# Performance work log

Hardware: AMD Instinct MI355X
Metric: run time of the kernel (lower is better)

## Reference

```python
import jax, jax.numpy as jnp
import numpy as np

D = 12       # series_dim
L = 1024     # series_length
N = 16       # batch
ADM = 64     # adm_dim
HID = 16     # hidden_size (d_model for gru)
E = 8        # datum_emb_size
OUT = 1      # output_dim
H = HID * D  # GRU hidden per direction = 192
FFH = 512    # PositionWiseFFN hidden


def setup_inputs() -> dict:
    key = jax.random.key(0)
    ks = jax.random.split(key, 20)
    def g(i, shape, s):
        return jax.random.normal(ks[i], shape, jnp.float32) * s
    sh = float(1.0 / np.sqrt(H))
    z = lambda *shape: jnp.zeros(shape, jnp.float32)
    inp = {
        'series': jax.random.normal(ks[0], (N, L, D), jnp.float32),
        'adm': jax.random.normal(ks[1], (N, ADM), jnp.float32),
        'mask': jax.random.randint(ks[2], (N, L, D), 0, 2, jnp.int32),
        'series_W': g(3, (D, E), 1.0),                       # per-channel Linear(1->8), no bias
        'mask_emb': g(4, (D + 1, E), 1.0).at[0].set(0.0),    # padding_idx=0
        'adm_W1': g(5, (HID, ADM), float(1.0 / np.sqrt(ADM))), 'adm_b1': z(HID),
        'adm_W2': g(6, (HID, HID), float(1.0 / np.sqrt(HID))), 'adm_b2': z(HID),
        'Wih0f': g(7, (3 * H, E * D), sh), 'Whh0f': g(8, (3 * H, H), sh), 'bih0f': z(3 * H), 'bhh0f': z(3 * H),
        'Wih0b': g(9, (3 * H, E * D), sh), 'Whh0b': g(10, (3 * H, H), sh), 'bih0b': z(3 * H), 'bhh0b': z(3 * H),
        'Wih1f': g(11, (3 * H, 2 * H), sh), 'Whh1f': g(12, (3 * H, H), sh), 'bih1f': z(3 * H), 'bhh1f': z(3 * H),
        'Wih1b': g(13, (3 * H, 2 * H), sh), 'Whh1b': g(14, (3 * H, H), sh), 'bih1b': z(3 * H), 'bhh1b': z(3 * H),
        'ffn_W1': g(15, (D, FFH, 3 * HID), float(1.0 / np.sqrt(3 * HID))), 'ffn_b1': z(D, FFH),
        'ln_g': jnp.ones((D, FFH), jnp.float32), 'ln_b': z(D, FFH),
        'ffn_W2': g(16, (D, OUT, FFH), float(1.0 / np.sqrt(FFH))), 'ffn_b2': z(D, OUT),
    }
    return inp


def _gru_dir(xp, Whh, bhh, reverse):
    # xp: [N, L, 3H] = x @ W_ih^T + b_ih precomputed for all timesteps
    Hs = Whh.shape[1]
    def step(h, x):
        gh = h @ Whh.T + bhh
        xr, xz, xn = jnp.split(x, 3, axis=-1)
        hr, hz, hn = jnp.split(gh, 3, axis=-1)
        r = jax.nn.sigmoid(xr + hr)
        zg = jax.nn.sigmoid(xz + hz)
        n = jnp.tanh(xn + r * hn)
        hnew = (1.0 - zg) * n + zg * h
        return hnew, hnew
    h0 = jnp.zeros((xp.shape[0], Hs), xp.dtype)
    _, hs = jax.lax.scan(step, h0, jnp.swapaxes(xp, 0, 1), reverse=reverse)
    return jnp.swapaxes(hs, 0, 1)


def reference(series, adm, mask, series_W, mask_emb, adm_W1, adm_b1, adm_W2, adm_b2,
              Wih0f, Whh0f, bih0f, bhh0f, Wih0b, Whh0b, bih0b, bhh0b,
              Wih1f, Whh1f, bih1f, bhh1f, Wih1b, Whh1b, bih1b, bhh1b,
              ffn_W1, ffn_b1, ln_g, ln_b, ffn_W2, ffn_b2):
    n, l, d = series.shape
    # adm MLP (dropouts are identity in eval)
    adm_out = jnp.maximum(adm @ adm_W1.T + adm_b1, 0.0) @ adm_W2.T + adm_b2  # [N, HID]
    # fused per-channel mask-embedding lookup + Linear(1->8) + add
    idx = mask * jnp.arange(1, d + 1, dtype=mask.dtype)          # [N,L,D]
    memb = mask_emb[idx]                                          # [N,L,D,E]
    semb = jnp.einsum('nld,de->nlde', series, series_W)           # [N,L,D,E]
    h = (memb + semb).reshape(n, l, d * E)                        # GRU input [N,L,96]
    # 2-layer bidirectional GRU
    layers = ((Wih0f, Whh0f, bih0f, bhh0f, Wih0b, Whh0b, bih0b, bhh0b),
              (Wih1f, Whh1f, bih1f, bhh1f, Wih1b, Whh1b, bih1b, bhh1b))
    for (Wf, Uf, bif, bhf, Wb, Ub, bib, bhb) in layers:
        fwd = _gru_dir(h @ Wf.T + bif, Uf, bhf, False)
        bwd = _gru_dir(h @ Wb.T + bib, Ub, bhb, True)
        h = jnp.concatenate([fwd, bwd], axis=-1)                  # [N,L,2H]
    # chunk rnn output into D slices of width 2H/D = 32
    r = h.reshape(n, l, d, (2 * H) // d)
    a = jnp.broadcast_to(adm_out[:, None, None, :], (n, l, d, adm_out.shape[-1]))
    feat = jnp.concatenate([r, a], axis=-1)                       # [N,L,D,3*HID]
    # per-channel PositionWiseFFN: Linear -> (Dropout) -> LayerNorm -> ReLU -> Linear
    hh = jnp.einsum('nldk,dhk->nldh', feat, ffn_W1) + ffn_b1      # [N,L,D,FFH]
    mu = hh.mean(axis=-1, keepdims=True)
    var = ((hh - mu) ** 2).mean(axis=-1, keepdims=True)
    hh = (hh - mu) / jnp.sqrt(var + 1e-5) * ln_g + ln_b
    hh = jnp.maximum(hh, 0.0)
    o = jnp.einsum('nldh,doh->nldo', hh, ffn_W2) + ffn_b2         # [N,L,D,OUT]
    return o.reshape(n, l, d * OUT)
```

## Files before the change

### kernel.cpp

```cpp
#include <hip/hip_runtime.h>
#include <math.h>


constexpr int N_   = 16;
constexpr int L_   = 1024;
constexpr int D_   = 12;
constexpr int E_   = 8;
constexpr int HID_ = 16;
constexpr int ADM_ = 64;
constexpr int H_   = 192;
constexpr int H3_  = 576;
constexpr int IN0_ = 96;
constexpr int IN1_ = 384;
constexpr int NL_  = N_ * L_;
constexpr int FFH_ = 512;

#define F4(p) (*(const float4*)(p))

typedef _Float16 half2v __attribute__((ext_vector_type(2)));
union U32H2 { unsigned int u; half2v h; };
union H16U { _Float16 f; unsigned short s; };

__device__ __forceinline__ float dot2acc(unsigned int wu, unsigned int hu, float acc) {
#if __has_builtin(__builtin_amdgcn_fdot2)
  U32H2 a, b; a.u = wu; b.u = hu;
  return __builtin_amdgcn_fdot2(a.h, b.h, acc, false);
#else
  U32H2 a, b; a.u = wu; b.u = hu;
  acc = fmaf((float)a.h.x, (float)b.h.x, acc);
  return fmaf((float)a.h.y, (float)b.h.y, acc);
#endif
}

__global__ void adm_mlp_kernel(const float* __restrict__ adm,
                               const float* __restrict__ W1, const float* __restrict__ b1,
                               const float* __restrict__ W2, const float* __restrict__ b2,
                               float* __restrict__ adm_out) {
  __shared__ float hid[N_][HID_];
  const int t = threadIdx.x;
  const int n = t >> 4, j = t & 15;
  float acc = b1[j];
  for (int k = 0; k < ADM_; ++k) acc = fmaf(adm[n * ADM_ + k], W1[j * ADM_ + k], acc);
  hid[n][j] = fmaxf(acc, 0.f);
  __syncthreads();
  float acc2 = b2[j];
  for (int k = 0; k < HID_; ++k) acc2 = fmaf(hid[n][k], W2[j * HID_ + k], acc2);
  adm_out[n * HID_ + j] = acc2;
}

__global__ void embed_kernel(const float* __restrict__ series, const int* __restrict__ mask,
                             const float* __restrict__ sW, const float* __restrict__ membW,
                             float* __restrict__ emb) {
  const int i = blockIdx.x * blockDim.x + threadIdx.x;
  if (i >= NL_ * IN0_) return;
  const int de = i % IN0_;
  const int nl = i / IN0_;
  const int d = de >> 3, e = de & 7;
  const float s = series[nl * D_ + d];
  const int   m = mask[nl * D_ + d];
  const int idx = m ? (d + 1) : 0;
  emb[i] = membW[idx * E_ + e] + s * sW[de];
}

__global__ void whh_pack16_kernel(const float* __restrict__ Whh, unsigned int* __restrict__ Wp) {
  const int o = blockIdx.x * blockDim.x + threadIdx.x;
  if (o >= H3_ * 96) return;
  const int c  = o & 3;
  const int j  = (o >> 2) % H3_;
  const int kc = (o >> 2) / H3_;
  const int k  = kc * 8 + c * 2;
  H16U lo, hi;
  lo.f = (_Float16)Whh[j * H_ + k];
  hi.f = (_Float16)Whh[j * H_ + k + 1];
  Wp[o] = (unsigned int)lo.s | ((unsigned int)hi.s << 16);
}

__global__ __launch_bounds__(256)
void xp_gemm_kernel(const float* __restrict__ A, const int K,
                    const float* __restrict__ Wf, const float* __restrict__ Wb,
                    const float* __restrict__ bf, const float* __restrict__ bb,
                    float* __restrict__ xp ) {
  constexpr int BM = 128, BN = 128, BK = 16, TM = 8, TN = 8;
  __shared__ float As[BK][BM + 4];
  __shared__ float Bs[BK][BN + 4];
  const int bm = blockIdx.x;
  const int bn = blockIdx.y;
  const int t = threadIdx.x;
  const int tx = t & 15, ty = t >> 4;
  const int row0 = bm * BM, col0 = bn * BN;
  float acc[TM][TN] = {};

  for (int k0 = 0; k0 < K; k0 += BK) {
    #pragma unroll
    for (int r = 0; r < 2; ++r) {
      const int li = t + r * 256;
      const int i = li >> 2;
      const int kc = (li & 3) << 2;
      float4 v = F4(A + (size_t)(row0 + i) * K + k0 + kc);
      As[kc + 0][i] = v.x; As[kc + 1][i] = v.y; As[kc + 2][i] = v.z; As[kc + 3][i] = v.w;
    }
    #pragma unroll
    for (int r = 0; r < 2; ++r) {
      const int li = t + r * 256;
      const int jj = li >> 2;
      const int kc = (li & 3) << 2;
      const int col = col0 + jj;
      const float* W = (col < H3_) ? Wf : Wb;
      const int wrow = (col < H3_) ? col : col - H3_;
      float4 v = F4(W + (size_t)wrow * K + k0 + kc);
      Bs[kc + 0][jj] = v.x; Bs[kc + 1][jj] = v.y; Bs[kc + 2][jj] = v.z; Bs[kc + 3][jj] = v.w;
    }
    __syncthreads();
    #pragma unroll
    for (int kk = 0; kk < BK; ++kk) {
      float a[TM], b[TN];
      const float4* a4 = (const float4*)&As[kk][ty * TM];
      const float4* b4 = (const float4*)&Bs[kk][tx * TN];
      float4 av0 = a4[0], av1 = a4[1], bv0 = b4[0], bv1 = b4[1];
      a[0]=av0.x; a[1]=av0.y; a[2]=av0.z; a[3]=av0.w; a[4]=av1.x; a[5]=av1.y; a[6]=av1.z; a[7]=av1.w;
      b[0]=bv0.x; b[1]=bv0.y; b[2]=bv0.z; b[3]=bv0.w; b[4]=bv1.x; b[5]=bv1.y; b[6]=bv1.z; b[7]=bv1.w;
      #pragma unroll
      for (int i = 0; i < TM; ++i)
        #pragma unroll
        for (int jq = 0; jq < TN; ++jq) acc[i][jq] = fmaf(a[i], b[jq], acc[i][jq]);
    }
    __syncthreads();
  }
  #pragma unroll
  for (int i = 0; i < TM; ++i) {
    const int row = row0 + ty * TM + i;
    #pragma unroll
    for (int jq = 0; jq < TN; ++jq) {
      const int col = col0 + tx * TN + jq;
      const int dir = (col >= H3_);
      const int jj = col - dir * H3_;
      const float bias = dir ? bb[jj] : bf[jj];
      xp[((size_t)dir * NL_ + row) * H3_ + jj] = acc[i][jq] + bias;
    }
  }
}

__global__ __launch_bounds__(H3_, 1)
void gru_scan_kernel(const float* __restrict__ xp,
                     const unsigned int* __restrict__ Wpf,
                     const unsigned int* __restrict__ Wpb,
                     const float* __restrict__ bhf,
                     const float* __restrict__ bhb,
                     float* __restrict__ hcat) {
  const int dir = blockIdx.x >> 4;
  const int n   = blockIdx.x & 15;
  const float* __restrict__ xpd = xp + ((size_t)dir * NL_ + (size_t)n * L_) * H3_;
  const unsigned int* __restrict__ Wp = dir ? Wpb : Wpf;
  const float* __restrict__ bh  = dir ? bhb : bhf;
  float* __restrict__ outd = hcat + (size_t)n * L_ * IN1_ + dir * H_;

  const int j = threadIdx.x;

  __shared__ __align__(16) unsigned int h16[96];
  __shared__ float gh_lds[H3_];
  __shared__ float xn_lds[H_];

  uint4 w[24];
  #pragma unroll
  for (int kc = 0; kc < 24; ++kc)
    w[kc] = ((const uint4*)Wp)[kc * H3_ + j];

  const float bj = bh[j];
  if (j < 96) h16[j] = 0u;
  float hprev = 0.f;
  __syncthreads();

  const uint4* __restrict__ h4 = (const uint4*)h16;
  const int ts = dir ? -1 : 1;
  int t = dir ? (L_ - 1) : 0;
  float xv = xpd[(size_t)t * H3_ + j];

  for (int tt = 0; tt < L_; ++tt) {
    float xvn = 0.f;
    if (tt + 1 < L_) xvn = xpd[(size_t)(t + ts) * H3_ + j];

    float a0 = bj, a1 = 0.f, a2 = 0.f, a3 = 0.f;
    #pragma unroll
    for (int kc = 0; kc < 24; ++kc) {
      uint4 hv = h4[kc];
      a0 = dot2acc(w[kc].x, hv.x, a0);
      a1 = dot2acc(w[kc].y, hv.y, a1);
      a2 = dot2acc(w[kc].z, hv.z, a2);
      a3 = dot2acc(w[kc].w, hv.w, a3);
    }
    float acc = (a0 + a1) + (a2 + a3);

    if (j < 2 * H_) acc += xv;
    gh_lds[j] = acc;
    if (j >= 2 * H_) xn_lds[j - 2 * H_] = xv;
    __syncthreads();

    if (j < H_) {
      const float r  = 1.f / (1.f + __expf(-gh_lds[j]));
      const float z  = 1.f / (1.f + __expf(-gh_lds[H_ + j]));
      const float nn = tanhf(xn_lds[j] + r * gh_lds[2 * H_ + j]);
      const float hnew = (1.f - z) * nn + z * hprev;
      hprev = hnew;
      H16U cv; cv.f = (_Float16)hnew;
      ((unsigned short*)h16)[j] = cv.s;
      outd[(size_t)t * IN1_ + j] = hnew;
    }
    __syncthreads();

    xv = xvn;
    t += ts;
  }
}

__global__ __launch_bounds__(256)
void ffn_kernel(const float* __restrict__ hcat, const float* __restrict__ adm_out,
                const float* __restrict__ W1, const float* __restrict__ b1,
                const float* __restrict__ lng, const float* __restrict__ lnb,
                const float* __restrict__ W2, const float* __restrict__ b2,
                float* __restrict__ out) {
  constexpr int FROWS = 8;
  const int d = blockIdx.y;
  const int row_base = blockIdx.x * 128;
  const int t = threadIdx.x;
  const int lane = t & 63, w = t >> 6;

  __shared__ __align__(16) float featL[FROWS][48];
  __shared__ __align__(16) float hhL[FROWS][FFH_];
  __shared__ float gL[FFH_], bLn[FFH_], w2L[FFH_], b1L[FFH_];

  for (int i = t; i < FFH_; i += 256) {
    gL[i]  = lng[d * FFH_ + i];
    bLn[i] = lnb[d * FFH_ + i];
    w2L[i] = W2[d * FFH_ + i];
    b1L[i] = b1[d * FFH_ + i];
  }
  float w1a[48], w1b[48];
  {
    const float* ra = W1 + ((size_t)d * FFH_ + t) * 48;
    const float* rb = W1 + ((size_t)d * FFH_ + 256 + t) * 48;
    #pragma unroll
    for (int kc = 0; kc < 12; ++kc) {
      float4 va = F4(ra + kc * 4);
      w1a[4*kc+0]=va.x; w1a[4*kc+1]=va.y; w1a[4*kc+2]=va.z; w1a[4*kc+3]=va.w;
      float4 vb = F4(rb + kc * 4);
      w1b[4*kc+0]=vb.x; w1b[4*kc+1]=vb.y; w1b[4*kc+2]=vb.z; w1b[4*kc+3]=vb.w;
    }
  }
  const float b2v = b2[d];
  __syncthreads();

  for (int c0 = 0; c0 < 128; c0 += FROWS) {
    for (int idx = t; idx < FROWS * 48; idx += 256) {
      const int r = idx / 48, k = idx % 48;
      const int row = row_base + c0 + r;
      float v;
      if (k < 32) v = hcat[(size_t)row * IN1_ + d * 32 + k];
      else        v = adm_out[(row >> 10) * HID_ + (k - 32)];
      featL[r][k] = v;
    }
    __syncthreads();
    float acc_a[FROWS] = {}, acc_b[FROWS] = {};
    #pragma unroll
    for (int r = 0; r < FROWS; ++r) {
      const float4* f4 = (const float4*)featL[r];
      #pragma unroll
      for (int kc = 0; kc < 12; ++kc) {
        float4 f = f4[kc];
        acc_a[r] = fmaf(w1a[4*kc+0], f.x, acc_a[r]);
        acc_a[r] = fmaf(w1a[4*kc+1], f.y, acc_a[r]);
        acc_a[r] = fmaf(w1a[4*kc+2], f.z, acc_a[r]);
        acc_a[r] = fmaf(w1a[4*kc+3], f.w, acc_a[r]);
        acc_b[r] = fmaf(w1b[4*kc+0], f.x, acc_b[r]);
        acc_b[r] = fmaf(w1b[4*kc+1], f.y, acc_b[r]);
        acc_b[r] = fmaf(w1b[4*kc+2], f.z, acc_b[r]);
        acc_b[r] = fmaf(w1b[4*kc+3], f.w, acc_b[r]);
      }
    }
    #pragma unroll
    for (int r = 0; r < FROWS; ++r) {
      hhL[r][t]       = acc_a[r] + b1L[t];
      hhL[r][t + 256] = acc_b[r] + b1L[t + 256];
    }
    __syncthreads();
    #pragma unroll
    for (int rr = 0; rr < 2; ++rr) {
      const int r = w + rr * 4;
      const float4* h4 = (const float4*)hhL[r];
      float4 x0 = h4[lane * 2], x1 = h4[lane * 2 + 1];
      float s = x0.x + x0.y + x0.z + x0.w + x1.x + x1.y + x1.z + x1.w;
      float q = x0.x*x0.x + x0.y*x0.y + x0.z*x0.z + x0.w*x0.w
              + x1.x*x1.x + x1.y*x1.y + x1.z*x1.z + x1.w*x1.w;
      #pragma unroll
      for (int m = 1; m < 64; m <<= 1) { s += __shfl_xor(s, m); q += __shfl_xor(q, m); }
      const float mu   = s * (1.f / FFH_);
      const float var  = q * (1.f / FFH_) - mu * mu;
      const float rstd = rsqrtf(var + 1e-5f);
      const int col = lane * 8;
      const float xs[8] = {x0.x, x0.y, x0.z, x0.w, x1.x, x1.y, x1.z, x1.w};
      float o = 0.f;
      #pragma unroll
      for (int i = 0; i < 8; ++i) {
        float v = (xs[i] - mu) * rstd * gL[col + i] + bLn[col + i];
        v = fmaxf(v, 0.f);
        o = fmaf(v, w2L[col + i], o);
      }
      #pragma unroll
      for (int m = 1; m < 64; m <<= 1) o += __shfl_xor(o, m);
      if (lane == 0) {
        const int row = row_base + c0 + r;
        out[(size_t)row * D_ + d] = o + b2v;
      }
    }
    __syncthreads();
  }
}

extern "C" void kernel_launch(void* const* d_in, const int* in_sizes, int n_in,
                              void* d_out, int out_size, void* d_ws, size_t ws_size,
                              hipStream_t stream) {
  const float* series = (const float*)d_in[0];
  const float* adm    = (const float*)d_in[1];
  const int*   mask   = (const int*)  d_in[2];
  const float* sW     = (const float*)d_in[3];
  const float* membW  = (const float*)d_in[4];
  const float* aW1    = (const float*)d_in[5];
  const float* ab1    = (const float*)d_in[6];
  const float* aW2    = (const float*)d_in[7];
  const float* ab2    = (const float*)d_in[8];
  const float* Wih0f  = (const float*)d_in[9];
  const float* Whh0f  = (const float*)d_in[10];
  const float* bih0f  = (const float*)d_in[11];
  const float* bhh0f  = (const float*)d_in[12];
  const float* Wih0b  = (const float*)d_in[13];
  const float* Whh0b  = (const float*)d_in[14];
  const float* bih0b  = (const float*)d_in[15];
  const float* bhh0b  = (const float*)d_in[16];
  const float* Wih1f  = (const float*)d_in[17];
  const float* Whh1f  = (const float*)d_in[18];
  const float* bih1f  = (const float*)d_in[19];
  const float* bhh1f  = (const float*)d_in[20];
  const float* Wih1b  = (const float*)d_in[21];
  const float* Whh1b  = (const float*)d_in[22];
  const float* bih1b  = (const float*)d_in[23];
  const float* bhh1b  = (const float*)d_in[24];
  const float* ffnW1  = (const float*)d_in[25];
  const float* ffnb1  = (const float*)d_in[26];
  const float* lng    = (const float*)d_in[27];
  const float* lnb    = (const float*)d_in[28];
  const float* ffnW2  = (const float*)d_in[29];
  const float* ffnb2  = (const float*)d_in[30];
  float* outp = (float*)d_out;

  float* ws      = (float*)d_ws;
  float* adm_out = ws;
  float* emb     = adm_out + 256;
  float* xp      = emb + (size_t)NL_ * IN0_;
  float* hcat    = xp + (size_t)2 * NL_ * H3_;
  unsigned int* wp0f = (unsigned int*)(hcat + (size_t)NL_ * IN1_);
  unsigned int* wp0b = wp0f + (size_t)H3_ * 96;
  unsigned int* wp1f = wp0b + (size_t)H3_ * 96;
  unsigned int* wp1b = wp1f + (size_t)H3_ * 96;

  adm_mlp_kernel<<<1, 256, 0, stream>>>(adm, aW1, ab1, aW2, ab2, adm_out);
  embed_kernel<<<(NL_ * IN0_) / 256, 256, 0, stream>>>(series, mask, sW, membW, emb);
  whh_pack16_kernel<<<(H3_ * 96) / 256, 256, 0, stream>>>(Whh0f, wp0f);
  whh_pack16_kernel<<<(H3_ * 96) / 256, 256, 0, stream>>>(Whh0b, wp0b);
  whh_pack16_kernel<<<(H3_ * 96) / 256, 256, 0, stream>>>(Whh1f, wp1f);
  whh_pack16_kernel<<<(H3_ * 96) / 256, 256, 0, stream>>>(Whh1b, wp1b);

  xp_gemm_kernel<<<dim3(NL_ / 128, (2 * H3_) / 128), 256, 0, stream>>>(
      emb, IN0_, Wih0f, Wih0b, bih0f, bih0b, xp);
  gru_scan_kernel<<<32, H3_, 0, stream>>>(xp, wp0f, wp0b, bhh0f, bhh0b, hcat);

  xp_gemm_kernel<<<dim3(NL_ / 128, (2 * H3_) / 128), 256, 0, stream>>>(
      hcat, IN1_, Wih1f, Wih1b, bih1f, bih1b, xp);
  gru_scan_kernel<<<32, H3_, 0, stream>>>(xp, wp1f, wp1b, bhh1f, bhh1b, hcat);

  ffn_kernel<<<dim3(NL_ / 128, D_), 256, 0, stream>>>(
      hcat, adm_out, ffnW1, ffnb1, lng, lnb, ffnW2, ffnb2, outp);
}
```

Baseline: 2.692 ms.

## Compute two GRU gate rows per thread in recurrent scan kernel

Each thread of the GRU scan now handles two rows of the recurrent matrix, holding both weight slices in registers. The block shrinks from 576 to 320 threads, of which 288 do the matvec. Fewer waves per step should cut synchronisation and scheduling overhead and let each shared-memory read of h feed twice as many dot products. In exchange each thread runs twice as many serial dot operations, register pressure roughly doubles to 192 weight registers, and 32 threads sit idle during the matvec.

```diff
diff --git a/kernel.cpp b/kernel.cpp
--- a/kernel.cpp
+++ b/kernel.cpp
@@ -140,7 +140,7 @@
   }
 }
 
-__global__ __launch_bounds__(H3_, 1)
+__global__ __launch_bounds__(320, 2)
 void gru_scan_kernel(const float* __restrict__ xp,
                      const unsigned int* __restrict__ Wpf,
                      const unsigned int* __restrict__ Wpb,
@@ -154,45 +154,67 @@
   const float* __restrict__ bh  = dir ? bhb : bhf;
   float* __restrict__ outd = hcat + (size_t)n * L_ * IN1_ + dir * H_;
 
-  const int j = threadIdx.x;
-
-  __shared__ __align__(16) unsigned int h16[96];
+  const int j  = threadIdx.x;
+  const int j2 = j + 288;
+  const bool act = (j < 288);
+
+  __shared__ __align__(16) unsigned int h16[128];
   __shared__ float gh_lds[H3_];
   __shared__ float xn_lds[H_];
 
-  uint4 w[24];
-  #pragma unroll
-  for (int kc = 0; kc < 24; ++kc)
-    w[kc] = ((const uint4*)Wp)[kc * H3_ + j];
-
-  const float bj = bh[j];
-  if (j < 96) h16[j] = 0u;
+  uint4 w1[24], w2[24];
+  if (act) {
+    #pragma unroll
+    for (int kc = 0; kc < 24; ++kc) {
+      w1[kc] = ((const uint4*)Wp)[kc * H3_ + j];
+      w2[kc] = ((const uint4*)Wp)[kc * H3_ + j2];
+    }
+  }
+  const float bj1 = act ? bh[j]  : 0.f;
+  const float bj2 = act ? bh[j2] : 0.f;
+  if (j < 128) h16[j] = 0u;
   float hprev = 0.f;
   __syncthreads();
 
   const uint4* __restrict__ h4 = (const uint4*)h16;
   const int ts = dir ? -1 : 1;
   int t = dir ? (L_ - 1) : 0;
-  float xv = xpd[(size_t)t * H3_ + j];
+  float xv1 = 0.f, xv2 = 0.f;
+  if (act) { xv1 = xpd[(size_t)t * H3_ + j]; xv2 = xpd[(size_t)t * H3_ + j2]; }
 
   for (int tt = 0; tt < L_; ++tt) {
-    float xvn = 0.f;
-    if (tt + 1 < L_) xvn = xpd[(size_t)(t + ts) * H3_ + j];
-
-    float a0 = bj, a1 = 0.f, a2 = 0.f, a3 = 0.f;
-    #pragma unroll
-    for (int kc = 0; kc < 24; ++kc) {
-      uint4 hv = h4[kc];
-      a0 = dot2acc(w[kc].x, hv.x, a0);
-      a1 = dot2acc(w[kc].y, hv.y, a1);
-      a2 = dot2acc(w[kc].z, hv.z, a2);
-      a3 = dot2acc(w[kc].w, hv.w, a3);
-    }
-    float acc = (a0 + a1) + (a2 + a3);
-
-    if (j < 2 * H_) acc += xv;
-    gh_lds[j] = acc;
-    if (j >= 2 * H_) xn_lds[j - 2 * H_] = xv;
+    float xn1 = 0.f, xn2 = 0.f;
+    if (act && tt + 1 < L_) {
+      xn1 = xpd[(size_t)(t + ts) * H3_ + j];
+      xn2 = xpd[(size_t)(t + ts) * H3_ + j2];
+    }
+
+    if (act) {
+      float a0 = bj1, a1 = 0.f, a2 = 0.f, a3 = 0.f;
+      float c0 = bj2, c1 = 0.f, c2 = 0.f, c3 = 0.f;
+      #pragma unroll
+      for (int kc = 0; kc < 24; ++kc) {
+        uint4 hv = h4[kc];
+        a0 = dot2acc(w1[kc].x, hv.x, a0);
+        a1 = dot2acc(w1[kc].y, hv.y, a1);
+        a2 = dot2acc(w1[kc].z, hv.z, a2);
+        a3 = dot2acc(w1[kc].w, hv.w, a3);
+        c0 = dot2acc(w2[kc].x, hv.x, c0);
+        c1 = dot2acc(w2[kc].y, hv.y, c1);
+        c2 = dot2acc(w2[kc].z, hv.z, c2);
+        c3 = dot2acc(w2[kc].w, hv.w, c3);
+      }
+      float acc1 = (a0 + a1) + (a2 + a3);
+      float acc2 = (c0 + c1) + (c2 + c3);
+
+      gh_lds[j] = acc1 + xv1;
+      if (j < 96) {
+        gh_lds[j2] = acc2 + xv2;
+      } else {
+        gh_lds[j2] = acc2;
+        xn_lds[j2 - 2 * H_] = xv2;
+      }
+    }
     __syncthreads();
 
     if (j < H_) {
@@ -207,7 +229,7 @@
     }
     __syncthreads();
 
-    xv = xvn;
+    xv1 = xn1; xv2 = xn2;
     t += ts;
   }
 }
@@ -370,11 +392,11 @@
 
   xp_gemm_kernel<<<dim3(NL_ / 128, (2 * H3_) / 128), 256, 0, stream>>>(
       emb, IN0_, Wih0f, Wih0b, bih0f, bih0b, xp);
-  gru_scan_kernel<<<32, H3_, 0, stream>>>(xp, wp0f, wp0b, bhh0f, bhh0b, hcat);
+  gru_scan_kernel<<<32, 320, 0, stream>>>(xp, wp0f, wp0b, bhh0f, bhh0b, hcat);
 
   xp_gemm_kernel<<<dim3(NL_ / 128, (2 * H3_) / 128), 256, 0, stream>>>(
       hcat, IN1_, Wih1f, Wih1b, bih1f, bih1b, xp);
-  gru_scan_kernel<<<32, H3_, 0, stream>>>(xp, wp1f, wp1b, bhh1f, bhh1b, hcat);
+  gru_scan_kernel<<<32, 320, 0, stream>>>(xp, wp1f, wp1b, bhh1f, bhh1b, hcat);
 
   ffn_kernel<<<dim3(NL_ / 128, D_), 256, 0, stream>>>(
       hcat, adm_out, ffnW1, ffnb1, lng, lnb, ffnW2, ffnb2, outp);
```

Measured after the change: 3.467 ms. 1.29x slower.

## Use MFMA-based batched GRU scan for layer-0 recurrence

Applied to the files above, without the earlier changes.

Adds a new recurrent scan kernel for the first GRU layer. Each block handles 4 batch rows per direction and computes h@Whh^T with 16x16x32 f16 MFMA instructions, using weights pre-packed into the MFMA fragment layout and held in registers. This replaces the per-sample dot2 scan, cutting the block count from 32 to 8 and reusing the weights across 4 sequences. The cost is that 12 of the 16 MFMA columns are wasted padding, the work runs on only 8 CUs, and two barriers are needed per step. Layer 1 keeps the old scan, now renamed.

```diff
diff --git a/kernel.cpp b/kernel.cpp
--- a/kernel.cpp
+++ b/kernel.cpp
@@ -18,8 +18,11 @@
 #define F4(p) (*(const float4*)(p))
 
 typedef _Float16 half2v __attribute__((ext_vector_type(2)));
+typedef _Float16 f16x8  __attribute__((ext_vector_type(8)));
+typedef float    f32x4  __attribute__((ext_vector_type(4)));
 union U32H2 { unsigned int u; half2v h; };
-union H16U { _Float16 f; unsigned short s; };
+union H16U  { _Float16 f; unsigned short s; };
+union FU    { uint4 u; f16x8 h; };
 
 __device__ __forceinline__ float dot2acc(unsigned int wu, unsigned int hu, float acc) {
 #if __has_builtin(__builtin_amdgcn_fdot2)
@@ -75,6 +78,21 @@
   Wp[o] = (unsigned int)lo.s | ((unsigned int)hi.s << 16);
 }
 
+__global__ void wmf_pack16_kernel(const float* __restrict__ Whh, unsigned int* __restrict__ Wp) {
+  const int o = blockIdx.x * blockDim.x + threadIdx.x;
+  if (o >= 216 * 256) return;
+  const int e2   = o & 3;
+  const int lane = (o >> 2) & 63;
+  const int tile = o >> 8;
+  const int jt = tile / 6, kc = tile % 6;
+  const int row = jt * 16 + (lane & 15);
+  const int k   = kc * 32 + (lane >> 4) * 8 + e2 * 2;
+  H16U lo, hi;
+  lo.f = (_Float16)Whh[row * H_ + k];
+  hi.f = (_Float16)Whh[row * H_ + k + 1];
+  Wp[o] = (unsigned int)lo.s | ((unsigned int)hi.s << 16);
+}
+
 __global__ __launch_bounds__(256)
 void xp_gemm_kernel(const float* __restrict__ A, const int K,
                     const float* __restrict__ Wf, const float* __restrict__ Wb,
@@ -140,13 +158,131 @@
   }
 }
 
+__global__ __launch_bounds__(512, 2)
+void gru_scan_mf(const float* __restrict__ xp,
+                 const unsigned int* __restrict__ WmfF,
+                 const unsigned int* __restrict__ WmfB,
+                 const float* __restrict__ bhf,
+                 const float* __restrict__ bhb,
+                 float* __restrict__ hcat) {
+  const int dir = blockIdx.x >> 2;
+  const int n0  = (blockIdx.x & 3) * 4;
+  const int tid = threadIdx.x, lane = tid & 63, wv = tid >> 6;
+  const uint4* __restrict__ Wm = (const uint4*)(dir ? WmfB : WmfF);
+  const float* __restrict__ bh = dir ? bhb : bhf;
+
+  __shared__ __align__(16) _Float16 hT[16][200];
+  __shared__ __align__(16) float    DL[4][592];
+
+  const int nt = (wv < 4) ? 5 : 4;
+  FU wf[5][6];
+  #pragma unroll
+  for (int s = 0; s < 5; ++s) {
+    if (s < nt) {
+      const int jt = wv + 8 * s;
+      #pragma unroll
+      for (int kc = 0; kc < 6; ++kc)
+        wf[s][kc].u = Wm[(jt * 6 + kc) * 64 + lane];
+    }
+  }
+
+  for (int i = tid; i < 1600; i += 512) ((unsigned int*)hT)[i] = 0u;
+
+  const int  b0 = tid & 3, i0 = tid >> 2;
+  const bool has1 = (tid < 256);
+  const int  b1 = (tid + 512) & 3;
+  const int  i1 = has1 ? ((tid + 512) >> 2) : 0;
+  const float bh0r = bh[i0], bh0z = bh[i0 + 192], bh0n = bh[i0 + 384];
+  const float bh1r = has1 ? bh[i1] : 0.f;
+  const float bh1z = has1 ? bh[i1 + 192] : 0.f;
+  const float bh1n = has1 ? bh[i1 + 384] : 0.f;
+  const float* __restrict__ xp0 = xp + ((size_t)dir * NL_ + (size_t)(n0 + b0) * L_) * H3_;
+  const float* __restrict__ xp1 = xp + ((size_t)dir * NL_ + (size_t)(n0 + b1) * L_) * H3_;
+  float* __restrict__ hc0 = hcat + (size_t)(n0 + b0) * L_ * IN1_ + dir * H_ + i0;
+  float* __restrict__ hc1 = hcat + (size_t)(n0 + b1) * L_ * IN1_ + dir * H_ + i1;
+
+  const int ts = dir ? -1 : 1;
+  int t = dir ? (L_ - 1) : 0;
+  float x0r = xp0[(size_t)t * H3_ + i0];
+  float x0z = xp0[(size_t)t * H3_ + i0 + 192];
+  float x0n = xp0[(size_t)t * H3_ + i0 + 384];
+  float x1r = 0.f, x1z = 0.f, x1n = 0.f;
+  if (has1) {
+    x1r = xp1[(size_t)t * H3_ + i1];
+    x1z = xp1[(size_t)t * H3_ + i1 + 192];
+    x1n = xp1[(size_t)t * H3_ + i1 + 384];
+  }
+  float h0p = 0.f, h1p = 0.f;
+  __syncthreads();
+
+  for (int tt = 0; tt < L_; ++tt) {
+    FU hb[6];
+    #pragma unroll
+    for (int kc = 0; kc < 6; ++kc)
+      hb[kc].h = *(const f16x8*)&hT[lane & 15][kc * 32 + (lane >> 4) * 8];
+
+    f32x4 acc[5];
+    #pragma unroll
+    for (int s = 0; s < 5; ++s) acc[s] = (f32x4){0.f, 0.f, 0.f, 0.f};
+    #pragma unroll
+    for (int kc = 0; kc < 6; ++kc) {
+      #pragma unroll
+      for (int s = 0; s < 5; ++s)
+        if (s < nt)
+          acc[s] = __builtin_amdgcn_mfma_f32_16x16x32_f16(wf[s][kc].h, hb[kc].h, acc[s], 0, 0, 0);
+    }
+
+    float y0r = 0.f, y0z = 0.f, y0n = 0.f, y1r = 0.f, y1z = 0.f, y1n = 0.f;
+    if (tt + 1 < L_) {
+      const size_t o = (size_t)(t + ts) * H3_;
+      y0r = xp0[o + i0]; y0z = xp0[o + i0 + 192]; y0n = xp0[o + i0 + 384];
+      if (has1) { y1r = xp1[o + i1]; y1z = xp1[o + i1 + 192]; y1n = xp1[o + i1 + 384]; }
+    }
+
+    if ((lane & 15) < 4) {
+      #pragma unroll
+      for (int s = 0; s < 5; ++s)
+        if (s < nt) {
+          const int jt = wv + 8 * s;
+          *(f32x4*)&DL[lane & 15][jt * 16 + (lane >> 4) * 4] = acc[s];
+        }
+    }
+    __syncthreads();
+
+    {
+      const float r  = 1.f / (1.f + __expf(-(x0r + DL[b0][i0]       + bh0r)));
+      const float z  = 1.f / (1.f + __expf(-(x0z + DL[b0][i0 + 192] + bh0z)));
+      const float nn = tanhf(x0n + r * (DL[b0][i0 + 384] + bh0n));
+      const float hn = (1.f - z) * nn + z * h0p;
+      h0p = hn;
+      H16U cv; cv.f = (_Float16)hn;
+      ((unsigned short*)&hT[b0][0])[i0] = cv.s;
+      hc0[(size_t)t * IN1_] = hn;
+    }
+    if (has1) {
+      const float r  = 1.f / (1.f + __expf(-(x1r + DL[b1][i1]       + bh1r)));
+      const float z  = 1.f / (1.f + __expf(-(x1z + DL[b1][i1 + 192] + bh1z)));
+      const float nn = tanhf(x1n + r * (DL[b1][i1 + 384] + bh1n));
+      const float hn = (1.f - z) * nn + z * h1p;
+      h1p = hn;
+      H16U cv; cv.f = (_Float16)hn;
+      ((unsigned short*)&hT[b1][0])[i1] = cv.s;
+      hc1[(size_t)t * IN1_] = hn;
+    }
+    __syncthreads();
+
+    x0r = y0r; x0z = y0z; x0n = y0n; x1r = y1r; x1z = y1z; x1n = y1n;
+    t += ts;
+  }
+}
+
 __global__ __launch_bounds__(H3_, 1)
-void gru_scan_kernel(const float* __restrict__ xp,
-                     const unsigned int* __restrict__ Wpf,
-                     const unsigned int* __restrict__ Wpb,
-                     const float* __restrict__ bhf,
-                     const float* __restrict__ bhb,
-                     float* __restrict__ hcat) {
+void gru_scan_r4(const float* __restrict__ xp,
+                 const unsigned int* __restrict__ Wpf,
+                 const unsigned int* __restrict__ Wpb,
+                 const float* __restrict__ bhf,
+                 const float* __restrict__ bhb,
+                 float* __restrict__ hcat) {
   const int dir = blockIdx.x >> 4;
   const int n   = blockIdx.x & 15;
   const float* __restrict__ xpd = xp + ((size_t)dir * NL_ + (size_t)n * L_) * H3_;
@@ -156,7 +292,7 @@
 
   const int j = threadIdx.x;
 
-  __shared__ __align__(16) unsigned int h16[96];
+  __shared__ __align__(16) unsigned int h16[128];
   __shared__ float gh_lds[H3_];
   __shared__ float xn_lds[H_];
 
@@ -166,7 +302,7 @@
     w[kc] = ((const uint4*)Wp)[kc * H3_ + j];
 
   const float bj = bh[j];
-  if (j < 96) h16[j] = 0u;
+  if (j < 128) h16[j] = 0u;
   float hprev = 0.f;
   __syncthreads();
 
@@ -356,25 +492,25 @@
   float* emb     = adm_out + 256;
   float* xp      = emb + (size_t)NL_ * IN0_;
   float* hcat    = xp + (size_t)2 * NL_ * H3_;
-  unsigned int* wp0f = (unsigned int*)(hcat + (size_t)NL_ * IN1_);
-  unsigned int* wp0b = wp0f + (size_t)H3_ * 96;
-  unsigned int* wp1f = wp0b + (size_t)H3_ * 96;
-  unsigned int* wp1b = wp1f + (size_t)H3_ * 96;
+  unsigned int* wmf0f = (unsigned int*)(hcat + (size_t)NL_ * IN1_);
+  unsigned int* wmf0b = wmf0f + (size_t)H3_ * 96;
+  unsigned int* wp1f  = wmf0b + (size_t)H3_ * 96;
+  unsigned int* wp1b  = wp1f + (size_t)H3_ * 96;
 
   adm_mlp_kernel<<<1, 256, 0, stream>>>(adm, aW1, ab1, aW2, ab2, adm_out);
   embed_kernel<<<(NL_ * IN0_) / 256, 256, 0, stream>>>(series, mask, sW, membW, emb);
-  whh_pack16_kernel<<<(H3_ * 96) / 256, 256, 0, stream>>>(Whh0f, wp0f);
-  whh_pack16_kernel<<<(H3_ * 96) / 256, 256, 0, stream>>>(Whh0b, wp0b);
+  wmf_pack16_kernel<<<(216 * 256) / 256, 256, 0, stream>>>(Whh0f, wmf0f);
+  wmf_pack16_kernel<<<(216 * 256) / 256, 256, 0, stream>>>(Whh0b, wmf0b);
   whh_pack16_kernel<<<(H3_ * 96) / 256, 256, 0, stream>>>(Whh1f, wp1f);
   whh_pack16_kernel<<<(H3_ * 96) / 256, 256, 0, stream>>>(Whh1b, wp1b);
 
   xp_gemm_kernel<<<dim3(NL_ / 128, (2 * H3_) / 128), 256, 0, stream>>>(
       emb, IN0_, Wih0f, Wih0b, bih0f, bih0b, xp);
-  gru_scan_kernel<<<32, H3_, 0, stream>>>(xp, wp0f, wp0b, bhh0f, bhh0b, hcat);
+  gru_scan_mf<<<8, 512, 0, stream>>>(xp, wmf0f, wmf0b, bhh0f, bhh0b, hcat);
 
   xp_gemm_kernel<<<dim3(NL_ / 128, (2 * H3_) / 128), 256, 0, stream>>>(
       hcat, IN1_, Wih1f, Wih1b, bih1f, bih1b, xp);
-  gru_scan_kernel<<<32, H3_, 0, stream>>>(xp, wp1f, wp1b, bhh1f, bhh1b, hcat);
+  gru_scan_r4<<<32, H3_, 0, stream>>>(xp, wp1f, wp1b, bhh1f, bhh1b, hcat);
 
   ffn_kernel<<<dim3(NL_ / 128, D_), 256, 0, stream>>>(
       hcat, adm_out, ffnW1, ffnb1, lng, lnb, ffnW2, ffnb2, outp);
```

Result: no change. 2.734 ms (+1.6%).
